# Kernel optimization log

Measured on AMD Instinct MI355X. Metric: run time of the kernel, lower is better.

## Reference

```python
import jax, jax.numpy as jnp
import numpy as np

VX, VY = 0.2, 0.2
X_OFFSET = VX / 2 + 0.0      # pc_range[0] = 0
Y_OFFSET = VY / 2 + (-40.0)  # pc_range[1] = -40
BN_EPS = 1e-3
IN_CH, OUT_CH = 9, 64


def setup_inputs() -> dict:
    key = jax.random.key(0)
    k1, k2, k3, k4 = jax.random.split(key, 4)
    bs, V, P = 2, 12000, 100
    features = jax.random.normal(k1, (bs, V, P, 4), dtype=jnp.float32)
    num_points = jax.random.randint(k2, (bs, V), 0, 100, dtype=jnp.int32)
    coors = jax.random.randint(k3, (bs, V, 4), 0, 352, dtype=jnp.int32)
    W = jax.random.normal(k4, (IN_CH, OUT_CH), dtype=jnp.float32) * 0.1
    gamma = jnp.ones((OUT_CH,), dtype=jnp.float32)
    beta = jnp.zeros((OUT_CH,), dtype=jnp.float32)
    return {"features": features, "num_points": num_points, "coors": coors,
            "W": W, "gamma": gamma, "beta": beta}


def reference(features, num_points, coors, W, gamma, beta):
    bs, V, P, _ = features.shape
    dt = features.dtype
    npf = num_points.astype(dt)

    # cluster features: offset from per-pillar mean of xyz
    points_mean = features[..., :3].sum(axis=2, keepdims=True) / jnp.maximum(npf, 1.0)[:, :, None, None]
    f_cluster = features[..., :3] - points_mean

    # center features: offset from pillar center (coors[...,2] = x idx, coors[...,1] = y idx)
    coors_f = coors.astype(dt)
    fcx = features[..., 0] - (coors_f[:, :, 2][:, :, None] * VX + X_OFFSET)
    fcy = features[..., 1] - (coors_f[:, :, 1][:, :, None] * VY + Y_OFFSET)
    f_center = jnp.stack([fcx, fcy], axis=-1)

    feats = jnp.concatenate([features, f_cluster, f_center], axis=-1)  # [bs,V,P,9]

    # padding mask over points in each pillar
    mask = (num_points[:, :, None] > jnp.arange(P)).astype(dt)[..., None]
    feats = feats * mask

    # PFNLayer (last layer): Linear(no bias) -> BatchNorm1d(train-mode stats) -> ReLU -> max over points
    x = jnp.einsum('bvpi,io->bvpo', feats, W)  # [bs,V,P,64]
    mean = x.mean(axis=(0, 1, 2))
    var = x.var(axis=(0, 1, 2))  # biased variance, as torch BN uses for normalization
    x = (x - mean) * jax.lax.rsqrt(var + BN_EPS) * gamma + beta
    x = jax.nn.relu(x)
    return x.max(axis=2)  # [bs,V,64]
```

## Files before the change

### kernel.cpp

```cpp
#include <hip/hip_runtime.h>
#include <math.h>

#define NP 100
#define NPILLAR 24000
#define OUT_CH 64
#define NTOTAL 2400000.0
#define VXc 0.2f
#define VYc 0.2f
#define XOFF 0.1f
#define YOFF (-39.9f)
#define BN_EPS 1e-3
#define G1 768
#define NW1 (G1 * 4)
#define G2 1024
#define NW2 (G2 * 4)

typedef __attribute__((ext_vector_type(8))) short bf16x8;
typedef __attribute__((ext_vector_type(16))) float f32x16;
typedef __attribute__((ext_vector_type(4))) unsigned int uint4v;

__device__ __forceinline__ unsigned int f2bf(float x) {
    unsigned int b = __builtin_bit_cast(unsigned int, x);
    b += 0x7FFFu + ((b >> 16) & 1u);
    return b >> 16;
}

__device__ __forceinline__ unsigned int pk2(float a, float b) {
    return f2bf(a) | (f2bf(b) << 16);
}

__device__ __forceinline__ void build_f(const float4 p, float mx, float my, float mz,
                                        float cx, float cy, float* f) {
    f[0] = p.x; f[1] = p.y; f[2] = p.z; f[3] = p.w;
    f[4] = p.x - mx; f[5] = p.y - my; f[6] = p.z - mz;
    f[7] = p.x - cx; f[8] = p.y - cy;
}

__device__ __forceinline__ void moments(float* s, const float* f) {
    int k = 9;
#pragma unroll
    for (int i = 0; i < 9; ++i) {
        s[i] += f[i];
#pragma unroll
        for (int j = i; j < 9; ++j) { s[k] = fmaf(f[i], f[j], s[k]); ++k; }
    }
}

__global__ __launch_bounds__(256, 4) void pfn_stats(
    const float4* __restrict__ feat, const int* __restrict__ npts,
    const int* __restrict__ coors, float4* __restrict__ meta,
    double* __restrict__ tot)
{
    const int tid = threadIdx.x;
    const int lane = tid & 63;
    const int wv = tid >> 6;
    const int gw = blockIdx.x * 4 + wv;

    float s[54];
#pragma unroll
    for (int i = 0; i < 54; ++i) s[i] = 0.f;

    for (int pv = gw; pv < NPILLAR; pv += NW1) {
        const float4* fp = feat + (size_t)pv * NP;
        float4 p0 = fp[lane];
        float4 p1 = (lane + 64 < NP) ? fp[lane + 64] : make_float4(0.f, 0.f, 0.f, 0.f);

        float sx = p0.x + p1.x, sy = p0.y + p1.y, sz = p0.z + p1.z;
#pragma unroll
        for (int off = 32; off; off >>= 1) {
            sx += __shfl_xor(sx, off);
            sy += __shfl_xor(sy, off);
            sz += __shfl_xor(sz, off);
        }
        int np_ = npts[pv];
        if (np_ > NP) np_ = NP;
        float inv = 1.f / fmaxf((float)np_, 1.f);
        float mx = sx * inv, my = sy * inv, mz = sz * inv;
        float cx = (float)coors[pv * 4 + 2] * VXc + XOFF;
        float cy = (float)coors[pv * 4 + 1] * VYc + YOFF;
        if (lane == 0) {
            meta[2 * pv]     = make_float4(mx, my, mz, __int_as_float(np_));
            meta[2 * pv + 1] = make_float4(cx, cy, 0.f, 0.f);
        }

        float f[9];
        if (lane < np_) {
            build_f(p0, mx, my, mz, cx, cy, f);
            moments(s, f);
        }
        if (lane + 64 < np_) {
            build_f(p1, mx, my, mz, cx, cy, f);
            moments(s, f);
        }
    }

#pragma unroll
    for (int i = 0; i < 54; ++i) {
#pragma unroll
        for (int off = 32; off; off >>= 1) s[i] += __shfl_xor(s[i], off);
    }
    __shared__ float red[4][54];
    if (lane == 0) {
#pragma unroll
        for (int i = 0; i < 54; ++i) red[wv][i] = s[i];
    }
    __syncthreads();
    if (tid < 54) {
        atomicAdd(&tot[tid],
                  (double)(red[0][tid] + red[1][tid] + red[2][tid] + red[3][tid]));
    }
}

__global__ __launch_bounds__(256, 4) void pfn_apply(
    const float4* __restrict__ feat, const float4* __restrict__ meta,
    const double* __restrict__ tot, const float* __restrict__ W,
    const float* __restrict__ gamma, const float* __restrict__ beta,
    float* __restrict__ out)
{
    const int tid = threadIdx.x;
    const int lane = tid & 63;
    const int wv = tid >> 6;
    const int gw = blockIdx.x * 4 + wv;

    __shared__ float sc_s[64], sh_s[64];

    if (tid < 64) {
        double w[9];
#pragma unroll
        for (int i = 0; i < 9; ++i) w[i] = (double)W[i * OUT_CH + tid];
        double mean = 0.0;
#pragma unroll
        for (int i = 0; i < 9; ++i) mean += tot[i] * w[i];
        mean /= NTOTAL;
        double ex2 = 0.0;
        int k = 9;
#pragma unroll
        for (int i = 0; i < 9; ++i) {
#pragma unroll
            for (int j = i; j < 9; ++j) {
                ex2 += (i == j ? 1.0 : 2.0) * tot[k] * w[i] * w[j];
                ++k;
            }
        }
        ex2 /= NTOTAL;
        double var = ex2 - mean * mean;
        double scale = (double)gamma[tid] / sqrt(var + BN_EPS);
        double shift = (double)beta[tid] - mean * scale;
        sc_s[tid] = (float)scale;
        sh_s[tid] = (float)shift;
    }
    __syncthreads();

    const int col = lane & 31;
    const int kbase = (lane >> 5) * 8;
    const bool lo = (lane < 32);
    const float scv0 = sc_s[col];
    const float scv1 = sc_s[col + 32];
    uint4v bu0, bu1;
#pragma unroll
    for (int i = 0; i < 4; ++i) {
        int k0 = kbase + 2 * i, k1 = kbase + 2 * i + 1;
        float a0 = (k0 < 9) ? W[k0 * OUT_CH + col] * scv0 : 0.f;
        float a1 = (k1 < 9) ? W[k1 * OUT_CH + col] * scv0 : 0.f;
        float b0 = (k0 < 9) ? W[k0 * OUT_CH + 32 + col] * scv1 : 0.f;
        float b1 = (k1 < 9) ? W[k1 * OUT_CH + 32 + col] * scv1 : 0.f;
        bu0[i] = pk2(a0, a1);
        bu1[i] = pk2(b0, b1);
    }
    const bf16x8 bfr0 = __builtin_bit_cast(bf16x8, bu0);
    const bf16x8 bfr1 = __builtin_bit_cast(bf16x8, bu1);
    f32x16 cz;
#pragma unroll
    for (int i = 0; i < 16; ++i) cz[i] = 0.f;
    const float sh = sh_s[lane];

    for (int pv = gw; pv < NPILLAR; pv += NW2) {
        const float4* fp = feat + (size_t)pv * NP;
        float4 p0 = fp[lane];
        float4 p1 = (lane + 64 < NP) ? fp[lane + 64] : make_float4(0.f, 0.f, 0.f, 0.f);
        float4 m1 = meta[2 * pv];
        float4 m2 = meta[2 * pv + 1];
        const float mx = m1.x, my = m1.y, mz = m1.z;
        const int np_ = __float_as_int(m1.w);
        const float cx = m2.x, cy = m2.y;

        unsigned int A[5], B[5];
        {
            float f[9];
            if (lane < np_) {
                build_f(p0, mx, my, mz, cx, cy, f);
                A[0] = pk2(f[0], f[1]); A[1] = pk2(f[2], f[3]);
                A[2] = pk2(f[4], f[5]); A[3] = pk2(f[6], f[7]);
                A[4] = pk2(f[8], 0.f);
            } else {
#pragma unroll
                for (int i = 0; i < 5; ++i) A[i] = 0u;
            }
            if (lane + 64 < np_) {
                build_f(p1, mx, my, mz, cx, cy, f);
                B[0] = pk2(f[0], f[1]); B[1] = pk2(f[2], f[3]);
                B[2] = pk2(f[4], f[5]); B[3] = pk2(f[6], f[7]);
                B[4] = pk2(f[8], 0.f);
            } else {
#pragma unroll
                for (int i = 0; i < 5; ++i) B[i] = 0u;
            }
        }

        float xm0 = 0.f, xm1 = 0.f;
        const int nmt = (np_ + 31) >> 5;

        for (int mt = 0; mt < nmt; ++mt) {
            const int src = ((mt & 1) << 5) + col;
            unsigned int w0, w1, w2, w3, w4;
            if (mt < 2) {
                w0 = __shfl((int)A[0], src); w1 = __shfl((int)A[1], src);
                w2 = __shfl((int)A[2], src); w3 = __shfl((int)A[3], src);
                w4 = __shfl((int)A[4], src);
            } else {
                w0 = __shfl((int)B[0], src); w1 = __shfl((int)B[1], src);
                w2 = __shfl((int)B[2], src); w3 = __shfl((int)B[3], src);
                w4 = __shfl((int)B[4], src);
            }
            uint4v av = {lo ? w0 : w4, lo ? w1 : 0u, lo ? w2 : 0u, lo ? w3 : 0u};
            bf16x8 afr = __builtin_bit_cast(bf16x8, av);

            f32x16 c0 = __builtin_amdgcn_mfma_f32_32x32x16_bf16(afr, bfr0, cz, 0, 0, 0);
#pragma unroll
            for (int r = 0; r < 16; r += 2)
                xm0 = fmaxf(xm0, fmaxf(c0[r], c0[r + 1]));
            f32x16 c1 = __builtin_amdgcn_mfma_f32_32x32x16_bf16(afr, bfr1, cz, 0, 0, 0);
#pragma unroll
            for (int r = 0; r < 16; r += 2)
                xm1 = fmaxf(xm1, fmaxf(c1[r], c1[r + 1]));
        }

        xm0 = fmaxf(xm0, __shfl_xor(xm0, 32));
        xm1 = fmaxf(xm1, __shfl_xor(xm1, 32));

        out[(size_t)pv * OUT_CH + lane] = fmaxf((lo ? xm0 : xm1) + sh, 0.f);
    }
}

extern "C" void kernel_launch(void* const* d_in, const int* in_sizes, int n_in,
                              void* d_out, int out_size, void* d_ws, size_t ws_size,
                              hipStream_t stream) {
    const float4* feat = (const float4*)d_in[0];
    const int* npts    = (const int*)d_in[1];
    const int* coors   = (const int*)d_in[2];
    const float* W     = (const float*)d_in[3];
    const float* gamma = (const float*)d_in[4];
    const float* beta  = (const float*)d_in[5];

    double* tot  = (double*)d_ws;
    float4* meta = (float4*)((char*)d_ws + 512);

    (void)hipMemsetAsync(tot, 0, 54 * sizeof(double), stream);
    pfn_stats<<<G1, 256, 0, stream>>>(feat, npts, coors, meta, tot);
    pfn_apply<<<G2, 256, 0, stream>>>(feat, meta, tot, W, gamma, beta, (float*)d_out);
}
```

Baseline: 57.50 us.

## Fold cluster/center offsets into weights and per-pillar bias column

The 9-feature linear map is rewritten algebraically. Raw xyz and intensity are multiplied by combined weights, and the mean and center offsets become a per-pillar bias that enters the MFMA as an extra K column driven by a constant 1.0 input. This removes per-point construction and packing of the 9 derived features and the shuffling of five words per tile, leaving three. The BN scale/shift setup is now done per lane in registers instead of through shared memory and a barrier, and the occupancy hint is dropped. Per-point rounding changes: raw coordinates and the pillar bias are rounded to bf16 separately instead of rounding the differences, which may hurt accuracy when coordinates are large relative to the offsets.

```diff
diff --git a/kernel.cpp b/kernel.cpp
--- a/kernel.cpp
+++ b/kernel.cpp
@@ -24,7 +24,6 @@
     b += 0x7FFFu + ((b >> 16) & 1u);
     return b >> 16;
 }
-
 __device__ __forceinline__ unsigned int pk2(float a, float b) {
     return f2bf(a) | (f2bf(b) << 16);
 }
@@ -111,7 +110,7 @@
     }
 }
 
-__global__ __launch_bounds__(256, 4) void pfn_apply(
+__global__ __launch_bounds__(256) void pfn_apply(
     const float4* __restrict__ feat, const float4* __restrict__ meta,
     const double* __restrict__ tot, const float* __restrict__ W,
     const float* __restrict__ gamma, const float* __restrict__ beta,
@@ -121,13 +120,14 @@
     const int lane = tid & 63;
     const int wv = tid >> 6;
     const int gw = blockIdx.x * 4 + wv;
-
-    __shared__ float sc_s[64], sh_s[64];
-
-    if (tid < 64) {
+    const int col = lane & 31;
+    const bool lo = (lane < 32);
+
+    float scl, shf;
+    {
         double w[9];
 #pragma unroll
-        for (int i = 0; i < 9; ++i) w[i] = (double)W[i * OUT_CH + tid];
+        for (int i = 0; i < 9; ++i) w[i] = (double)W[i * OUT_CH + lane];
         double mean = 0.0;
 #pragma unroll
         for (int i = 0; i < 9; ++i) mean += tot[i] * w[i];
@@ -144,35 +144,35 @@
         }
         ex2 /= NTOTAL;
         double var = ex2 - mean * mean;
-        double scale = (double)gamma[tid] / sqrt(var + BN_EPS);
-        double shift = (double)beta[tid] - mean * scale;
-        sc_s[tid] = (float)scale;
-        sh_s[tid] = (float)shift;
-    }
-    __syncthreads();
-
-    const int col = lane & 31;
-    const int kbase = (lane >> 5) * 8;
-    const bool lo = (lane < 32);
-    const float scv0 = sc_s[col];
-    const float scv1 = sc_s[col + 32];
-    uint4v bu0, bu1;
-#pragma unroll
-    for (int i = 0; i < 4; ++i) {
-        int k0 = kbase + 2 * i, k1 = kbase + 2 * i + 1;
-        float a0 = (k0 < 9) ? W[k0 * OUT_CH + col] * scv0 : 0.f;
-        float a1 = (k1 < 9) ? W[k1 * OUT_CH + col] * scv0 : 0.f;
-        float b0 = (k0 < 9) ? W[k0 * OUT_CH + 32 + col] * scv1 : 0.f;
-        float b1 = (k1 < 9) ? W[k1 * OUT_CH + 32 + col] * scv1 : 0.f;
-        bu0[i] = pk2(a0, a1);
-        bu1[i] = pk2(b0, b1);
-    }
-    const bf16x8 bfr0 = __builtin_bit_cast(bf16x8, bu0);
-    const bf16x8 bfr1 = __builtin_bit_cast(bf16x8, bu1);
+        double scaled = (double)gamma[lane] / sqrt(var + BN_EPS);
+        scl = (float)scaled;
+        shf = (float)((double)beta[lane] - mean * scaled);
+    }
+
+    float w0f = W[0 * OUT_CH + lane], w1f = W[1 * OUT_CH + lane];
+    float w2f = W[2 * OUT_CH + lane], w3f = W[3 * OUT_CH + lane];
+    float w4f = W[4 * OUT_CH + lane], w5f = W[5 * OUT_CH + lane];
+    float w6f = W[6 * OUT_CH + lane], w7f = W[7 * OUT_CH + lane];
+    float w8f = W[8 * OUT_CH + lane];
+    float we0 = (w0f + w4f + w7f) * scl;
+    float we1 = (w1f + w5f + w8f) * scl;
+    float we2 = (w2f + w6f) * scl;
+    float we3 = w3f * scl;
+    float u4 = w4f * scl, u5 = w5f * scl, u6 = w6f * scl;
+    float u7 = w7f * scl, u8 = w8f * scl;
+
+    float a0 = __shfl(we0, col),      a1 = __shfl(we1, col);
+    float a2 = __shfl(we2, col),      a3 = __shfl(we3, col);
+    float b0 = __shfl(we0, col + 32), b1 = __shfl(we1, col + 32);
+    float b2 = __shfl(we2, col + 32), b3 = __shfl(we3, col + 32);
+    const unsigned B0w0 = lo ? pk2(a0, a1) : 0u;
+    const unsigned B0w1 = lo ? pk2(a2, a3) : 0u;
+    const unsigned B1w0 = lo ? pk2(b0, b1) : 0u;
+    const unsigned B1w1 = lo ? pk2(b2, b3) : 0u;
+
     f32x16 cz;
 #pragma unroll
     for (int i = 0; i < 16; ++i) cz[i] = 0.f;
-    const float sh = sh_s[lane];
 
     for (int pv = gw; pv < NPILLAR; pv += NW2) {
         const float4* fp = feat + (size_t)pv * NP;
@@ -180,49 +180,38 @@
         float4 p1 = (lane + 64 < NP) ? fp[lane + 64] : make_float4(0.f, 0.f, 0.f, 0.f);
         float4 m1 = meta[2 * pv];
         float4 m2 = meta[2 * pv + 1];
-        const float mx = m1.x, my = m1.y, mz = m1.z;
         const int np_ = __float_as_int(m1.w);
-        const float cx = m2.x, cy = m2.y;
-
-        unsigned int A[5], B[5];
-        {
-            float f[9];
-            if (lane < np_) {
-                build_f(p0, mx, my, mz, cx, cy, f);
-                A[0] = pk2(f[0], f[1]); A[1] = pk2(f[2], f[3]);
-                A[2] = pk2(f[4], f[5]); A[3] = pk2(f[6], f[7]);
-                A[4] = pk2(f[8], 0.f);
-            } else {
-#pragma unroll
-                for (int i = 0; i < 5; ++i) A[i] = 0u;
-            }
-            if (lane + 64 < np_) {
-                build_f(p1, mx, my, mz, cx, cy, f);
-                B[0] = pk2(f[0], f[1]); B[1] = pk2(f[2], f[3]);
-                B[2] = pk2(f[4], f[5]); B[3] = pk2(f[6], f[7]);
-                B[4] = pk2(f[8], 0.f);
-            } else {
-#pragma unroll
-                for (int i = 0; i < 5; ++i) B[i] = 0u;
-            }
-        }
+
+        float bsc = -(m1.x * u4 + m1.y * u5 + m1.z * u6 + m2.x * u7 + m2.y * u8);
+        unsigned bbf = f2bf(bsc);
+        unsigned bhi = (unsigned)__shfl((int)bbf, col + 32);
+        uint4v bv0 = {B0w0, B0w1, lo ? bbf : 0u, 0u};
+        uint4v bv1 = {B1w0, B1w1, lo ? bhi : 0u, 0u};
+        bf16x8 bfr0 = __builtin_bit_cast(bf16x8, bv0);
+        bf16x8 bfr1 = __builtin_bit_cast(bf16x8, bv1);
+
+        bool v0 = lane < np_, v1 = (lane + 64) < np_;
+        unsigned Ar0 = v0 ? pk2(p0.x, p0.y) : 0u;
+        unsigned Ar1 = v0 ? pk2(p0.z, p0.w) : 0u;
+        unsigned Ar2 = v0 ? 0x3F80u : 0u;
+        unsigned Br0 = v1 ? pk2(p1.x, p1.y) : 0u;
+        unsigned Br1 = v1 ? pk2(p1.z, p1.w) : 0u;
+        unsigned Br2 = v1 ? 0x3F80u : 0u;
 
         float xm0 = 0.f, xm1 = 0.f;
         const int nmt = (np_ + 31) >> 5;
 
         for (int mt = 0; mt < nmt; ++mt) {
             const int src = ((mt & 1) << 5) + col;
-            unsigned int w0, w1, w2, w3, w4;
+            unsigned w0_, w1_, w2_;
             if (mt < 2) {
-                w0 = __shfl((int)A[0], src); w1 = __shfl((int)A[1], src);
-                w2 = __shfl((int)A[2], src); w3 = __shfl((int)A[3], src);
-                w4 = __shfl((int)A[4], src);
+                w0_ = __shfl((int)Ar0, src); w1_ = __shfl((int)Ar1, src);
+                w2_ = __shfl((int)Ar2, src);
             } else {
-                w0 = __shfl((int)B[0], src); w1 = __shfl((int)B[1], src);
-                w2 = __shfl((int)B[2], src); w3 = __shfl((int)B[3], src);
-                w4 = __shfl((int)B[4], src);
+                w0_ = __shfl((int)Br0, src); w1_ = __shfl((int)Br1, src);
+                w2_ = __shfl((int)Br2, src);
             }
-            uint4v av = {lo ? w0 : w4, lo ? w1 : 0u, lo ? w2 : 0u, lo ? w3 : 0u};
+            uint4v av = {lo ? w0_ : 0u, lo ? w1_ : 0u, lo ? w2_ : 0u, 0u};
             bf16x8 afr = __builtin_bit_cast(bf16x8, av);
 
             f32x16 c0 = __builtin_amdgcn_mfma_f32_32x32x16_bf16(afr, bfr0, cz, 0, 0, 0);
@@ -238,7 +227,7 @@
         xm0 = fmaxf(xm0, __shfl_xor(xm0, 32));
         xm1 = fmaxf(xm1, __shfl_xor(xm1, 32));
 
-        out[(size_t)pv * OUT_CH + lane] = fmaxf((lo ? xm0 : xm1) + sh, 0.f);
+        out[(size_t)pv * OUT_CH + lane] = fmaxf((lo ? xm0 : xm1) + shf, 0.f);
     }
 }
 
```

Result: no change. 57.74 us (+0.4%).
